# Kernel tuning notes

Hardware: AMD Instinct MI355X
Metric: run time of the kernel (lower is better)

## Reference

```python
import jax, jax.numpy as jnp
import numpy as np

B, T, C = 4, 2048, 1024
N_HEAD = 16
HEAD = C // N_HEAD  # 64


def _rope_tables(T, dim, base=10000.0):
    inv_freq = 1.0 / (base ** (jnp.arange(0, dim, 2, dtype=jnp.float32) / dim))
    t = jnp.arange(T, dtype=jnp.float32)
    freqs = jnp.einsum('i,j->ij', t, inv_freq)           # [T, dim/2]
    emb = jnp.concatenate([freqs, freqs], axis=-1)        # [T, dim]
    return jnp.cos(emb), jnp.sin(emb)                     # each [T, dim]


def _rotate_half(x):
    x1, x2 = x[..., : x.shape[-1] // 2], x[..., x.shape[-1] // 2:]
    return jnp.concatenate([-x2, x1], axis=-1)


def setup_inputs() -> dict:
    key = jax.random.key(0)
    ks = jax.random.split(key, 4)
    x = jax.random.normal(ks[0], (B, T, C), dtype=jnp.float32)
    w_attn = jax.random.normal(ks[1], (C, 3 * C), dtype=jnp.float32) * (1.0 / np.sqrt(C))
    b_attn = jnp.zeros((3 * C,), dtype=jnp.float32)
    w_proj = jax.random.normal(ks[2], (C, C), dtype=jnp.float32) * (1.0 / np.sqrt(C))
    b_proj = jnp.zeros((C,), dtype=jnp.float32)
    return {"x": x, "w_attn": w_attn, "b_attn": b_attn, "w_proj": w_proj, "b_proj": b_proj}


def reference(x, w_attn, b_attn, w_proj, b_proj):
    Bx, Tx, Cx = x.shape
    qkv = x @ w_attn + b_attn                             # [B,T,3C]
    q, k, v = jnp.split(qkv, 3, axis=-1)
    # [B,T,C] -> [B,H,T,hd]
    def to_heads(t):
        return t.reshape(Bx, Tx, N_HEAD, HEAD).transpose(0, 2, 1, 3)
    q, k, v = to_heads(q), to_heads(k), to_heads(v)
    cos, sin = _rope_tables(Tx, HEAD)                     # [T,hd]
    cos = cos[None, None, :, :]
    sin = sin[None, None, :, :]
    q = q * cos + _rotate_half(q) * sin
    k = k * cos + _rotate_half(k) * sin
    scale = 1.0 / np.sqrt(HEAD)
    att = jnp.einsum('bhqd,bhkd->bhqk', q, k) * scale     # [B,H,T,T]
    causal = jnp.tril(jnp.ones((Tx, Tx), dtype=bool))
    att = jnp.where(causal[None, None], att, -jnp.inf)
    att = jax.nn.softmax(att, axis=-1)
    y = jnp.einsum('bhqk,bhkd->bhqd', att, v)             # [B,H,T,hd]
    y = y.transpose(0, 2, 1, 3).reshape(Bx, Tx, Cx)
    return y @ w_proj + b_proj
```

## Files before the change

### kernel.cpp

```cpp
#include <hip/hip_runtime.h>

#define B_  4
#define T_  2048
#define C_  1024
#define NH_ 16
#define HD_ 64
#define BT_ (B_*T_)
#define N3C (3*C_)

typedef _Float16 f16;
typedef _Float16 half8 __attribute__((ext_vector_type(8)));
typedef _Float16 half4 __attribute__((ext_vector_type(4)));
typedef float f32x4 __attribute__((ext_vector_type(4)));

__device__ __forceinline__ void gld16(const f16* g, f16* l) {
  __builtin_amdgcn_global_load_lds(
      (const __attribute__((address_space(1))) unsigned int*)g,
      (__attribute__((address_space(3))) unsigned int*)l, 16, 0, 0);
}

__global__ __launch_bounds__(256) void prep(
    const float* __restrict__ X, f16* __restrict__ X16,
    const float* __restrict__ Wa, f16* __restrict__ Wta,
    const float* __restrict__ Wp, f16* __restrict__ Wtp,
    float2* __restrict__ cs)
{
  __shared__ float Ls[64][65];
  const int tid = threadIdx.x;
  const int blk = blockIdx.x;
  if (blk < 4096) {
    const int i = blk * 256 + tid;
    const float4 a = ((const float4*)X)[i * 2];
    const float4 b = ((const float4*)X)[i * 2 + 1];
    half8 hx;
    hx[0] = (f16)a.x; hx[1] = (f16)a.y; hx[2] = (f16)a.z; hx[3] = (f16)a.w;
    hx[4] = (f16)b.x; hx[5] = (f16)b.y; hx[6] = (f16)b.z; hx[7] = (f16)b.w;
    ((half8*)X16)[i] = hx;
    return;
  }
  if (blk >= 5120) {
    const int i = (blk - 5120) * 256 + tid;
    const int f = i & 31, t = i >> 5;
    const float inv = expf(-(2.0f * (float)f / 64.0f) * 9.210340371976184f);
    float sn, cn;
    sincosf((float)t * inv, &sn, &cn);
    cs[i] = make_float2(cn, sn);
    return;
  }
  const float* W; f16* Wt; int N, i2;
  if (blk < 4864) { W = Wa; Wt = Wta; N = N3C; i2 = blk - 4096; }
  else            { W = Wp; Wt = Wtp; N = C_;  i2 = blk - 4864; }
  const int nblk = N >> 6;
  const int n0 = (i2 % nblk) * 64, k0 = (i2 / nblk) * 64;
#pragma unroll
  for (int j = 0; j < 4; ++j) {
    const int idx = j * 256 + tid;
    const int r = idx >> 4, c = (idx & 15) * 4;
    const float4 w = *(const float4*)(W + (size_t)(k0 + r) * N + n0 + c);
    Ls[r][c + 0] = w.x; Ls[r][c + 1] = w.y; Ls[r][c + 2] = w.z; Ls[r][c + 3] = w.w;
  }
  __syncthreads();
#pragma unroll
  for (int j = 0; j < 2; ++j) {
    const int idx = j * 256 + tid;
    const int r = idx >> 3, c = (idx & 7) * 8;
    half8 hw;
#pragma unroll
    for (int u = 0; u < 8; ++u) hw[u] = (f16)Ls[c + u][r];
    *(half8*)(Wt + (size_t)(n0 + r) * C_ + k0 + c) = hw;
  }
}

__global__ __launch_bounds__(256) void gemm_qkv(
    const f16* __restrict__ A, const f16* __restrict__ Bt,
    const float* __restrict__ bias, const float2* __restrict__ cs,
    f16* __restrict__ Qo, f16* __restrict__ Ko, f16* __restrict__ Vt_g)
{
  __shared__ f16 As[128 * 64];
  __shared__ f16 Bs[128 * 64];
  const int tid  = threadIdx.x;
  const int row0 = blockIdx.y * 128;
  const int col0 = blockIdx.x * 128;
  const int wave = tid >> 6, lane = tid & 63;
  const int l = lane & 15, quad = lane >> 4;
  const int wm = wave >> 1, wn = wave & 1;
  const int sr = tid >> 3;
  const int scs = ((tid & 7) ^ (sr & 7)) * 8;
  const int lq7 = l & 7;

  f32x4 acc[4][4];
#pragma unroll
  for (int mi = 0; mi < 4; ++mi)
#pragma unroll
    for (int ni = 0; ni < 4; ++ni) acc[mi][ni] = (f32x4)0.0f;

  for (int k0 = 0; k0 < C_; k0 += 64) {
    __syncthreads();
#pragma unroll
    for (int p = 0; p < 4; ++p) {
      const int r = p * 32 + sr;
      gld16(A  + (size_t)(row0 + r) * C_ + k0 + scs, &As[p * 2048 + tid * 8]);
      gld16(Bt + (size_t)(col0 + r) * C_ + k0 + scs, &Bs[p * 2048 + tid * 8]);
    }
    __syncthreads();

#pragma unroll
    for (int s = 0; s < 2; ++s) {
      half8 af[4], bf[4];
#pragma unroll
      for (int mi = 0; mi < 4; ++mi)
        af[mi] = *(const half8*)&As[(wm * 64 + mi * 16 + l) * 64 + ((((s << 2) | quad) ^ lq7) << 3)];
#pragma unroll
      for (int ni = 0; ni < 4; ++ni)
        bf[ni] = *(const half8*)&Bs[(wn * 64 + ni * 16 + l) * 64 + ((((s << 2) | quad) ^ lq7) << 3)];
#pragma unroll
      for (int mi = 0; mi < 4; ++mi)
#pragma unroll
        for (int ni = 0; ni < 4; ++ni)
          acc[mi][ni] = __builtin_amdgcn_mfma_f32_16x16x32_f16(af[mi], bf[ni], acc[mi][ni], 0, 0, 0);
    }
  }

  const int region = col0 >> 10;
  const int colw = col0 + wn * 64;
  const int h = (colw & 1023) >> 6;
  if (region < 2) {
    f16* dst = (region == 0) ? Qo : Ko;
    const float qs = (region == 0) ? 0.18033688f : 1.0f;
#pragma unroll
    for (int mi = 0; mi < 4; ++mi) {
#pragma unroll
      for (int r = 0; r < 4; ++r) {
        const int gm = row0 + wm * 64 + mi * 16 + quad * 4 + r;
        const int b = gm >> 11, t = gm & (T_ - 1);
        const size_t base = ((size_t)(b * NH_ + h) * T_ + t) * HD_;
        const float2* csrow = cs + t * 32;
#pragma unroll
        for (int ni = 0; ni < 2; ++ni) {
          const int d = ni * 16 + l;
          const float2 c2 = csrow[d];
          const float x1 = acc[mi][ni][r]     + bias[colw + d];
          const float x2 = acc[mi][ni + 2][r] + bias[colw + d + 32];
          dst[base + d]      = (f16)((x1 * c2.x - x2 * c2.y) * qs);
          dst[base + d + 32] = (f16)((x2 * c2.x + x1 * c2.y) * qs);
        }
      }
    }
  } else {
#pragma unroll
    for (int mi = 0; mi < 4; ++mi) {
      const int t0 = row0 + wm * 64 + mi * 16 + quad * 4;
      const int b = t0 >> 11, t = t0 & (T_ - 1);
#pragma unroll
      for (int ni = 0; ni < 4; ++ni) {
        const int d = ni * 16 + l;
        const float bs = bias[colw + d];
        half4 o;
#pragma unroll
        for (int r = 0; r < 4; ++r) o[r] = (f16)(acc[mi][ni][r] + bs);
        *(half4*)(Vt_g + ((size_t)((b * NH_ + h) * HD_ + d)) * T_ + t) = o;
      }
    }
  }
}

__global__ __launch_bounds__(256) void attn_mfma(
    const f16* __restrict__ Qg, const f16* __restrict__ Kg,
    const f16* __restrict__ Vt_g, f16* __restrict__ Y)
{
  __shared__ f16 Ks[2][64 * 64];
  __shared__ f16 Vt[2][64 * 64];
  const int tid  = threadIdx.x;
  const int qt   = 15 - (blockIdx.x >> 6);
  const int bh   = blockIdx.x & 63;
  const int b    = bh >> 4, h = bh & 15;
  const int wave = tid >> 6, lane = tid & 63;
  const int l    = lane & 15, quad = lane >> 4;
  const int lq7  = l & 7;
  int qrow[2];
  qrow[0] = qt * 128 + wave * 16 + l;
  qrow[1] = qrow[0] + 64;

  half8 qf[2][2];
#pragma unroll
  for (int u = 0; u < 2; ++u) {
    const f16* qp = Qg + ((size_t)bh * T_ + qrow[u]) * HD_;
#pragma unroll
    for (int s = 0; s < 2; ++s)
      qf[u][s] = *(const half8*)(qp + s * 32 + quad * 8);
  }

  f32x4 O[2][4];
#pragma unroll
  for (int u = 0; u < 2; ++u)
#pragma unroll
    for (int mi = 0; mi < 4; ++mi) O[u][mi] = (f32x4)0.0f;
  float l_run[2] = {0.f, 0.f};

  const f16* kbase  = Kg   + (size_t)bh * T_ * HD_;
  const f16* vtbase = Vt_g + (size_t)bh * HD_ * T_;
  const int r0 = tid >> 3, cc = tid & 7;

  const int nkt = 2 * qt + 2;
  half8 hk[2], hv[2];
#pragma unroll
  for (int i = 0; i < 2; ++i) {
    const int r = i * 32 + r0;
    hk[i] = *(const half8*)(kbase + (size_t)r * HD_ + cc * 8);
    hv[i] = *(const half8*)(vtbase + (size_t)r * T_ + cc * 8);
  }

  for (int kt = 0; kt < nkt; ++kt) {
    f16* KsB = Ks[kt & 1];
    f16* VtB = Vt[kt & 1];
#pragma unroll
    for (int i = 0; i < 2; ++i) {
      const int r = i * 32 + r0;
      const int cst = ((cc ^ (r & 7)) << 3);
      *(half8*)&KsB[r * 64 + cst] = hk[i];
      *(half8*)&VtB[r * 64 + cst] = hv[i];
    }
    __syncthreads();
    if (kt + 1 < nkt) {
#pragma unroll
      for (int i = 0; i < 2; ++i) {
        const int r = i * 32 + r0;
        hk[i] = *(const half8*)(kbase + (size_t)((kt + 1) * 64 + r) * HD_ + cc * 8);
        hv[i] = *(const half8*)(vtbase + (size_t)r * T_ + (kt + 1) * 64 + cc * 8);
      }
    }

    f32x4 St[2][4];
#pragma unroll
    for (int u = 0; u < 2; ++u)
#pragma unroll
      for (int st = 0; st < 4; ++st) St[u][st] = (f32x4)0.0f;
#pragma unroll
    for (int st = 0; st < 4; ++st) {
#pragma unroll
      for (int s = 0; s < 2; ++s) {
        const int row = st * 16 + l;
        const half8 af = *(const half8*)&KsB[row * 64 + ((((s << 2) | quad) ^ lq7) << 3)];
#pragma unroll
        for (int u = 0; u < 2; ++u)
          St[u][st] = __builtin_amdgcn_mfma_f32_16x16x32_f16(af, qf[u][s], St[u][st], 0, 0, 0);
      }
    }

    const bool domask = (kt >= 2 * qt);
    const int k0 = kt * 64;
    half4 pf[2][4];
#pragma unroll
    for (int u = 0; u < 2; ++u) {
      float psum = 0.f;
#pragma unroll
      for (int st = 0; st < 4; ++st) {
        float pv[4];
#pragma unroll
        for (int r = 0; r < 4; ++r) {
          float x = St[u][st][r];
          if (domask) {
            const int key = k0 + st * 16 + quad * 4 + r;
            if (key > qrow[u]) x = -1e9f;
          }
          const float ev = exp2f(x);
          pv[r] = ev;
          psum += ev;
        }
        pf[u][st][0] = (f16)pv[0]; pf[u][st][1] = (f16)pv[1];
        pf[u][st][2] = (f16)pv[2]; pf[u][st][3] = (f16)pv[3];
      }
      l_run[u] += psum;
    }

#pragma unroll
    for (int mi = 0; mi < 4; ++mi) {
      const int row = mi * 16 + l;
#pragma unroll
      for (int ki = 0; ki < 4; ++ki) {
        const int kch = (ki << 1) | (quad >> 1);
        const half4 vf = *(const half4*)&VtB[row * 64 + ((kch ^ lq7) << 3) + ((quad & 1) << 2)];
#pragma unroll
        for (int u = 0; u < 2; ++u)
          O[u][mi] = __builtin_amdgcn_mfma_f32_16x16x16f16(vf, pf[u][ki], O[u][mi], 0, 0, 0);
      }
    }
  }

#pragma unroll
  for (int u = 0; u < 2; ++u) {
    float lt = l_run[u];
    lt += __shfl_xor(lt, 16);
    lt += __shfl_xor(lt, 32);
    const float inv = 1.0f / lt;
    f16* yp = Y + ((size_t)(b * T_) + qrow[u]) * C_ + h * 64;
#pragma unroll
    for (int mi = 0; mi < 4; ++mi) {
      half4 o;
      o[0] = (f16)(O[u][mi][0] * inv); o[1] = (f16)(O[u][mi][1] * inv);
      o[2] = (f16)(O[u][mi][2] * inv); o[3] = (f16)(O[u][mi][3] * inv);
      *(half4*)(yp + mi * 16 + quad * 4) = o;
    }
  }
}

__global__ __launch_bounds__(256) void gemm_proj(
    const f16* __restrict__ A, const f16* __restrict__ Bt,
    const float* __restrict__ bias, float* __restrict__ Out)
{
  __shared__ f16 As[128 * 64];
  __shared__ f16 Bs[128 * 64];
  const int tid  = threadIdx.x;
  const int row0 = blockIdx.y * 128;
  const int col0 = blockIdx.x * 128;
  const int wave = tid >> 6, lane = tid & 63;
  const int l = lane & 15, quad = lane >> 4;
  const int wm = wave >> 1, wn = wave & 1;
  const int sr = tid >> 3;
  const int scs = ((tid & 7) ^ (sr & 7)) * 8;
  const int lq7 = l & 7;

  f32x4 acc[4][4];
#pragma unroll
  for (int mi = 0; mi < 4; ++mi)
#pragma unroll
    for (int ni = 0; ni < 4; ++ni) acc[mi][ni] = (f32x4)0.0f;

  for (int k0 = 0; k0 < C_; k0 += 64) {
    __syncthreads();
#pragma unroll
    for (int p = 0; p < 4; ++p) {
      const int r = p * 32 + sr;
      gld16(A  + (size_t)(row0 + r) * C_ + k0 + scs, &As[p * 2048 + tid * 8]);
      gld16(Bt + (size_t)(col0 + r) * C_ + k0 + scs, &Bs[p * 2048 + tid * 8]);
    }
    __syncthreads();

#pragma unroll
    for (int s = 0; s < 2; ++s) {
      half8 af[4], bf[4];
#pragma unroll
      for (int mi = 0; mi < 4; ++mi)
        af[mi] = *(const half8*)&As[(wm * 64 + mi * 16 + l) * 64 + ((((s << 2) | quad) ^ lq7) << 3)];
#pragma unroll
      for (int ni = 0; ni < 4; ++ni)
        bf[ni] = *(const half8*)&Bs[(wn * 64 + ni * 16 + l) * 64 + ((((s << 2) | quad) ^ lq7) << 3)];
#pragma unroll
      for (int mi = 0; mi < 4; ++mi)
#pragma unroll
        for (int ni = 0; ni < 4; ++ni)
          acc[mi][ni] = __builtin_amdgcn_mfma_f32_16x16x32_f16(af[mi], bf[ni], acc[mi][ni], 0, 0, 0);
    }
  }

#pragma unroll
  for (int mi = 0; mi < 4; ++mi) {
#pragma unroll
    for (int ni = 0; ni < 4; ++ni) {
#pragma unroll
      for (int r = 0; r < 4; ++r) {
        const int gm = row0 + wm * 64 + mi * 16 + quad * 4 + r;
        const int n  = col0 + wn * 64 + ni * 16 + l;
        Out[(size_t)gm * C_ + n] = acc[mi][ni][r] + bias[n];
      }
    }
  }
}

extern "C" void kernel_launch(void* const* d_in, const int* in_sizes, int n_in,
                              void* d_out, int out_size, void* d_ws, size_t ws_size,
                              hipStream_t stream) {
  const float* x      = (const float*)d_in[0];
  const float* w_attn = (const float*)d_in[1];
  const float* b_attn = (const float*)d_in[2];
  const float* w_proj = (const float*)d_in[3];
  const float* b_proj = (const float*)d_in[4];
  float* out = (float*)d_out;

  const size_t elems = (size_t)BT_ * C_;
  f16* x16 = (f16*)d_ws;
  f16* wta = x16 + elems;
  f16* wtp = wta + (size_t)N3C * C_;
  f16* q   = wtp + (size_t)C_ * C_;
  f16* k   = q + elems;
  f16* vt  = k + elems;
  f16* y   = vt + elems;
  float2* cs = (float2*)(y + elems);

  prep<<<dim3(5376), 256, 0, stream>>>(x, x16, w_attn, wta, w_proj, wtp, cs);
  gemm_qkv<<<dim3(N3C / 128, BT_ / 128), 256, 0, stream>>>(x16, wta, b_attn, cs, q, k, vt);
  attn_mfma<<<dim3(16 * 64), 256, 0, stream>>>(q, k, vt, y);
  gemm_proj<<<dim3(C_ / 128, BT_ / 128), 256, 0, stream>>>(y, wtp, b_proj, out);
}
```

Baseline: 272.3 us.

## Pair complementary 64-row query tiles per block for causal load balance

Each attention block now handles two 64-row query tiles (tiles pr and 31-pr) in sequence instead of one 128-row tile, so every block does about the same number of causal key tiles. Block indices are remapped so consecutive blocks spread across different (batch, head) pairs, likely with XCD placement in mind. In exchange, each loaded K/V tile now feeds 64 queries instead of 128, which doubles the K/V reloads and halves the MFMA work per LDS read, and a barrier is added between the two passes.

```diff
diff --git a/kernel.cpp b/kernel.cpp
--- a/kernel.cpp
+++ b/kernel.cpp
@@ -171,134 +171,126 @@
   __shared__ f16 Ks[2][64 * 64];
   __shared__ f16 Vt[2][64 * 64];
   const int tid  = threadIdx.x;
-  const int qt   = 15 - (blockIdx.x >> 6);
-  const int bh   = blockIdx.x & 63;
+  const int w    = (blockIdx.x & 7) * 128 + (blockIdx.x >> 3);
+  const int bh   = w >> 4;
+  const int pr   = w & 15;
   const int b    = bh >> 4, h = bh & 15;
   const int wave = tid >> 6, lane = tid & 63;
   const int l    = lane & 15, quad = lane >> 4;
   const int lq7  = l & 7;
-  int qrow[2];
-  qrow[0] = qt * 128 + wave * 16 + l;
-  qrow[1] = qrow[0] + 64;
-
-  half8 qf[2][2];
-#pragma unroll
-  for (int u = 0; u < 2; ++u) {
-    const f16* qp = Qg + ((size_t)bh * T_ + qrow[u]) * HD_;
-#pragma unroll
-    for (int s = 0; s < 2; ++s)
-      qf[u][s] = *(const half8*)(qp + s * 32 + quad * 8);
-  }
-
-  f32x4 O[2][4];
-#pragma unroll
-  for (int u = 0; u < 2; ++u)
-#pragma unroll
-    for (int mi = 0; mi < 4; ++mi) O[u][mi] = (f32x4)0.0f;
-  float l_run[2] = {0.f, 0.f};
+  const int r0   = tid >> 3, cc = tid & 7;
 
   const f16* kbase  = Kg   + (size_t)bh * T_ * HD_;
   const f16* vtbase = Vt_g + (size_t)bh * HD_ * T_;
-  const int r0 = tid >> 3, cc = tid & 7;
-
-  const int nkt = 2 * qt + 2;
-  half8 hk[2], hv[2];
-#pragma unroll
-  for (int i = 0; i < 2; ++i) {
-    const int r = i * 32 + r0;
-    hk[i] = *(const half8*)(kbase + (size_t)r * HD_ + cc * 8);
-    hv[i] = *(const half8*)(vtbase + (size_t)r * T_ + cc * 8);
-  }
-
-  for (int kt = 0; kt < nkt; ++kt) {
-    f16* KsB = Ks[kt & 1];
-    f16* VtB = Vt[kt & 1];
+
+  const int qts[2] = { 31 - pr, pr };
+
+#pragma unroll 1
+  for (int pass = 0; pass < 2; ++pass) {
+    const int qt   = qts[pass];
+    const int nkt  = qt + 1;
+    const int qrow = qt * 64 + wave * 16 + l;
+
+    half8 qf[2];
+    {
+      const f16* qp = Qg + ((size_t)bh * T_ + qrow) * HD_;
+      qf[0] = *(const half8*)(qp + quad * 8);
+      qf[1] = *(const half8*)(qp + 32 + quad * 8);
+    }
+
+    f32x4 O[4];
+#pragma unroll
+    for (int mi = 0; mi < 4; ++mi) O[mi] = (f32x4)0.0f;
+    float l_run = 0.f;
+
+    half8 hk[2], hv[2];
 #pragma unroll
     for (int i = 0; i < 2; ++i) {
       const int r = i * 32 + r0;
-      const int cst = ((cc ^ (r & 7)) << 3);
-      *(half8*)&KsB[r * 64 + cst] = hk[i];
-      *(half8*)&VtB[r * 64 + cst] = hv[i];
-    }
-    __syncthreads();
-    if (kt + 1 < nkt) {
+      hk[i] = *(const half8*)(kbase + (size_t)r * HD_ + cc * 8);
+      hv[i] = *(const half8*)(vtbase + (size_t)r * T_ + cc * 8);
+    }
+
+    if (pass == 1) __syncthreads();
+
+    for (int kt = 0; kt < nkt; ++kt) {
+      f16* KsB = Ks[kt & 1];
+      f16* VtB = Vt[kt & 1];
 #pragma unroll
       for (int i = 0; i < 2; ++i) {
         const int r = i * 32 + r0;
-        hk[i] = *(const half8*)(kbase + (size_t)((kt + 1) * 64 + r) * HD_ + cc * 8);
-        hv[i] = *(const half8*)(vtbase + (size_t)r * T_ + (kt + 1) * 64 + cc * 8);
-      }
-    }
-
-    f32x4 St[2][4];
-#pragma unroll
-    for (int u = 0; u < 2; ++u)
-#pragma unroll
-      for (int st = 0; st < 4; ++st) St[u][st] = (f32x4)0.0f;
-#pragma unroll
-    for (int st = 0; st < 4; ++st) {
-#pragma unroll
-      for (int s = 0; s < 2; ++s) {
-        const int row = st * 16 + l;
-        const half8 af = *(const half8*)&KsB[row * 64 + ((((s << 2) | quad) ^ lq7) << 3)];
-#pragma unroll
-        for (int u = 0; u < 2; ++u)
-          St[u][st] = __builtin_amdgcn_mfma_f32_16x16x32_f16(af, qf[u][s], St[u][st], 0, 0, 0);
-      }
-    }
-
-    const bool domask = (kt >= 2 * qt);
-    const int k0 = kt * 64;
-    half4 pf[2][4];
-#pragma unroll
-    for (int u = 0; u < 2; ++u) {
+        const int cst = ((cc ^ (r & 7)) << 3);
+        *(half8*)&KsB[r * 64 + cst] = hk[i];
+        *(half8*)&VtB[r * 64 + cst] = hv[i];
+      }
+      __syncthreads();
+      if (kt + 1 < nkt) {
+#pragma unroll
+        for (int i = 0; i < 2; ++i) {
+          const int r = i * 32 + r0;
+          hk[i] = *(const half8*)(kbase + (size_t)((kt + 1) * 64 + r) * HD_ + cc * 8);
+          hv[i] = *(const half8*)(vtbase + (size_t)r * T_ + (kt + 1) * 64 + cc * 8);
+        }
+      }
+
+      f32x4 St[4];
+#pragma unroll
+      for (int st = 0; st < 4; ++st) St[st] = (f32x4)0.0f;
+#pragma unroll
+      for (int st = 0; st < 4; ++st) {
+#pragma unroll
+        for (int s = 0; s < 2; ++s) {
+          const int row = st * 16 + l;
+          const half8 af = *(const half8*)&KsB[row * 64 + ((((s << 2) | quad) ^ lq7) << 3)];
+          St[st] = __builtin_amdgcn_mfma_f32_16x16x32_f16(af, qf[s], St[st], 0, 0, 0);
+        }
+      }
+
+      const bool domask = (kt == qt);
+      const int k0 = kt * 64;
+      half4 pf[4];
       float psum = 0.f;
 #pragma unroll
       for (int st = 0; st < 4; ++st) {
         float pv[4];
 #pragma unroll
         for (int r = 0; r < 4; ++r) {
-          float x = St[u][st][r];
+          float x = St[st][r];
           if (domask) {
             const int key = k0 + st * 16 + quad * 4 + r;
-            if (key > qrow[u]) x = -1e9f;
+            if (key > qrow) x = -1e9f;
           }
           const float ev = exp2f(x);
           pv[r] = ev;
           psum += ev;
         }
-        pf[u][st][0] = (f16)pv[0]; pf[u][st][1] = (f16)pv[1];
-        pf[u][st][2] = (f16)pv[2]; pf[u][st][3] = (f16)pv[3];
-      }
-      l_run[u] += psum;
-    }
-
-#pragma unroll
-    for (int mi = 0; mi < 4; ++mi) {
-      const int row = mi * 16 + l;
-#pragma unroll
-      for (int ki = 0; ki < 4; ++ki) {
-        const int kch = (ki << 1) | (quad >> 1);
-        const half4 vf = *(const half4*)&VtB[row * 64 + ((kch ^ lq7) << 3) + ((quad & 1) << 2)];
-#pragma unroll
-        for (int u = 0; u < 2; ++u)
-          O[u][mi] = __builtin_amdgcn_mfma_f32_16x16x16f16(vf, pf[u][ki], O[u][mi], 0, 0, 0);
-      }
-    }
-  }
-
-#pragma unroll
-  for (int u = 0; u < 2; ++u) {
-    float lt = l_run[u];
+        pf[st][0] = (f16)pv[0]; pf[st][1] = (f16)pv[1];
+        pf[st][2] = (f16)pv[2]; pf[st][3] = (f16)pv[3];
+      }
+      l_run += psum;
+
+#pragma unroll
+      for (int mi = 0; mi < 4; ++mi) {
+        const int row = mi * 16 + l;
+#pragma unroll
+        for (int ki = 0; ki < 4; ++ki) {
+          const int kch = (ki << 1) | (quad >> 1);
+          const half4 vf = *(const half4*)&VtB[row * 64 + ((kch ^ lq7) << 3) + ((quad & 1) << 2)];
+          O[mi] = __builtin_amdgcn_mfma_f32_16x16x16f16(vf, pf[ki], O[mi], 0, 0, 0);
+        }
+      }
+    }
+
+    float lt = l_run;
     lt += __shfl_xor(lt, 16);
     lt += __shfl_xor(lt, 32);
     const float inv = 1.0f / lt;
-    f16* yp = Y + ((size_t)(b * T_) + qrow[u]) * C_ + h * 64;
+    f16* yp = Y + ((size_t)(b * T_) + qrow) * C_ + h * 64;
 #pragma unroll
     for (int mi = 0; mi < 4; ++mi) {
       half4 o;
-      o[0] = (f16)(O[u][mi][0] * inv); o[1] = (f16)(O[u][mi][1] * inv);
-      o[2] = (f16)(O[u][mi][2] * inv); o[3] = (f16)(O[u][mi][3] * inv);
+      o[0] = (f16)(O[mi][0] * inv); o[1] = (f16)(O[mi][1] * inv);
+      o[2] = (f16)(O[mi][2] * inv); o[3] = (f16)(O[mi][3] * inv);
       *(half4*)(yp + mi * 16 + quad * 4) = o;
     }
   }
@@ -389,6 +381,6 @@
 
   prep<<<dim3(5376), 256, 0, stream>>>(x, x16, w_attn, wta, w_proj, wtp, cs);
   gemm_qkv<<<dim3(N3C / 128, BT_ / 128), 256, 0, stream>>>(x16, wta, b_attn, cs, q, k, vt);
-  attn_mfma<<<dim3(16 * 64), 256, 0, stream>>>(q, k, vt, y);
+  attn_mfma<<<dim3(1024), 256, 0, stream>>>(q, k, vt, y);
   gemm_proj<<<dim3(C_ / 128, BT_ / 128), 256, 0, stream>>>(y, wtp, b_proj, out);
 }
```

New measurement: 278.7 us. 1.02x slower.

## Pair complementary causal query tiles per block to balance attention work

Applied to the files above, without the earlier changes.

Each attention block now handles two 64-row query tiles, pr and 31-pr, instead of one contiguous 128-row tile. This gives every block the same number of key tiles, and the second tile's MFMAs are skipped once past its causal limit. Block indices are also remapped with an XCD-style interleave (blockIdx&7) so blocks from the same head are grouped. This targets load imbalance and tail effects from causal masking, at the cost of extra branching inside the loop and lower Q-tile reuse in later iterations.

```diff
diff --git a/kernel.cpp b/kernel.cpp
--- a/kernel.cpp
+++ b/kernel.cpp
@@ -171,23 +171,27 @@
   __shared__ f16 Ks[2][64 * 64];
   __shared__ f16 Vt[2][64 * 64];
   const int tid  = threadIdx.x;
-  const int qt   = 15 - (blockIdx.x >> 6);
-  const int bh   = blockIdx.x & 63;
+  const int w    = (blockIdx.x & 7) * 128 + (blockIdx.x >> 3);
+  const int bh   = w >> 4;
+  const int pr   = w & 15;
+  const int qta  = 31 - pr;
+  const int qtb  = pr;
   const int b    = bh >> 4, h = bh & 15;
   const int wave = tid >> 6, lane = tid & 63;
   const int l    = lane & 15, quad = lane >> 4;
   const int lq7  = l & 7;
+  const int r0   = tid >> 3, cc = tid & 7;
+
   int qrow[2];
-  qrow[0] = qt * 128 + wave * 16 + l;
-  qrow[1] = qrow[0] + 64;
+  qrow[0] = qta * 64 + wave * 16 + l;
+  qrow[1] = qtb * 64 + wave * 16 + l;
 
   half8 qf[2][2];
 #pragma unroll
   for (int u = 0; u < 2; ++u) {
     const f16* qp = Qg + ((size_t)bh * T_ + qrow[u]) * HD_;
-#pragma unroll
-    for (int s = 0; s < 2; ++s)
-      qf[u][s] = *(const half8*)(qp + s * 32 + quad * 8);
+    qf[u][0] = *(const half8*)(qp + quad * 8);
+    qf[u][1] = *(const half8*)(qp + 32 + quad * 8);
   }
 
   f32x4 O[2][4];
@@ -199,9 +203,8 @@
 
   const f16* kbase  = Kg   + (size_t)bh * T_ * HD_;
   const f16* vtbase = Vt_g + (size_t)bh * HD_ * T_;
-  const int r0 = tid >> 3, cc = tid & 7;
-
-  const int nkt = 2 * qt + 2;
+
+  const int nkt = qta + 1;
   half8 hk[2], hv[2];
 #pragma unroll
   for (int i = 0; i < 2; ++i) {
@@ -211,6 +214,7 @@
   }
 
   for (int kt = 0; kt < nkt; ++kt) {
+    const bool dual = (kt <= qtb);
     f16* KsB = Ks[kt & 1];
     f16* VtB = Vt[kt & 1];
 #pragma unroll
@@ -241,17 +245,18 @@
       for (int s = 0; s < 2; ++s) {
         const int row = st * 16 + l;
         const half8 af = *(const half8*)&KsB[row * 64 + ((((s << 2) | quad) ^ lq7) << 3)];
-#pragma unroll
-        for (int u = 0; u < 2; ++u)
-          St[u][st] = __builtin_amdgcn_mfma_f32_16x16x32_f16(af, qf[u][s], St[u][st], 0, 0, 0);
-      }
-    }
-
-    const bool domask = (kt >= 2 * qt);
+        St[0][st] = __builtin_amdgcn_mfma_f32_16x16x32_f16(af, qf[0][s], St[0][st], 0, 0, 0);
+        if (dual)
+          St[1][st] = __builtin_amdgcn_mfma_f32_16x16x32_f16(af, qf[1][s], St[1][st], 0, 0, 0);
+      }
+    }
+
     const int k0 = kt * 64;
     half4 pf[2][4];
 #pragma unroll
     for (int u = 0; u < 2; ++u) {
+      if (u == 1 && !dual) continue;
+      const bool domask = (kt == (u == 0 ? qta : qtb));
       float psum = 0.f;
 #pragma unroll
       for (int st = 0; st < 4; ++st) {
@@ -280,9 +285,9 @@
       for (int ki = 0; ki < 4; ++ki) {
         const int kch = (ki << 1) | (quad >> 1);
         const half4 vf = *(const half4*)&VtB[row * 64 + ((kch ^ lq7) << 3) + ((quad & 1) << 2)];
-#pragma unroll
-        for (int u = 0; u < 2; ++u)
-          O[u][mi] = __builtin_amdgcn_mfma_f32_16x16x16f16(vf, pf[u][ki], O[u][mi], 0, 0, 0);
+        O[0][mi] = __builtin_amdgcn_mfma_f32_16x16x16f16(vf, pf[0][ki], O[0][mi], 0, 0, 0);
+        if (dual)
+          O[1][mi] = __builtin_amdgcn_mfma_f32_16x16x16f16(vf, pf[1][ki], O[1][mi], 0, 0, 0);
       }
     }
   }
@@ -389,6 +394,6 @@
 
   prep<<<dim3(5376), 256, 0, stream>>>(x, x16, w_attn, wta, w_proj, wtp, cs);
   gemm_qkv<<<dim3(N3C / 128, BT_ / 128), 256, 0, stream>>>(x16, wta, b_attn, cs, q, k, vt);
-  attn_mfma<<<dim3(16 * 64), 256, 0, stream>>>(q, k, vt, y);
+  attn_mfma<<<dim3(1024), 256, 0, stream>>>(q, k, vt, y);
   gemm_proj<<<dim3(C_ / 128, BT_ / 128), 256, 0, stream>>>(y, wtp, b_proj, out);
 }
```

Measured after the change: 306.3 us. 1.13x slower.

## Pair causal query tiles per attention block and stage V-transpose stores through LDS

Applied to the files above, without the earlier changes.

The attention kernel now launches 512 blocks, and each block handles two query tiles (qt and 15-qt) one after the other. Every block therefore does the same amount of causal work, which removes the tail caused by unequal blocks. Block indices are also remapped so that blocks sharing a batch-head are spread out. In the QKV GEMM, the V-transposed output is written to a swizzled shared-memory tile first and then stored to global memory as coalesced 16-byte rows, instead of scattered 8-byte writes. The cost is an extra LDS round trip and barriers in the V path, plus fewer, longer attention blocks, which may lower occupancy and latency hiding.

```diff
diff --git a/kernel.cpp b/kernel.cpp
--- a/kernel.cpp
+++ b/kernel.cpp
@@ -76,8 +76,9 @@
     const float* __restrict__ bias, const float2* __restrict__ cs,
     f16* __restrict__ Qo, f16* __restrict__ Ko, f16* __restrict__ Vt_g)
 {
-  __shared__ f16 As[128 * 64];
-  __shared__ f16 Bs[128 * 64];
+  __shared__ f16 S[16384];
+  f16* As = S;
+  f16* Bs = S + 8192;
   const int tid  = threadIdx.x;
   const int row0 = blockIdx.y * 128;
   const int col0 = blockIdx.x * 128;
@@ -147,10 +148,12 @@
       }
     }
   } else {
+    __syncthreads();
+    const int bloc  = row0 >> 11;
+    const int tbase = row0 & (T_ - 1);
 #pragma unroll
     for (int mi = 0; mi < 4; ++mi) {
-      const int t0 = row0 + wm * 64 + mi * 16 + quad * 4;
-      const int b = t0 >> 11, t = t0 & (T_ - 1);
+      const int t_loc = wm * 64 + mi * 16 + quad * 4;
 #pragma unroll
       for (int ni = 0; ni < 4; ++ni) {
         const int d = ni * 16 + l;
@@ -158,8 +161,21 @@
         half4 o;
 #pragma unroll
         for (int r = 0; r < 4; ++r) o[r] = (f16)(acc[mi][ni][r] + bs);
-        *(half4*)(Vt_g + ((size_t)((b * NH_ + h) * HD_ + d)) * T_ + t) = o;
-      }
+        const int ts = t_loc ^ ((d & 15) << 3);
+        *(half4*)&S[wn * 8192 + d * 128 + ts] = o;
+      }
+    }
+    __syncthreads();
+#pragma unroll
+    for (int j = 0; j < 8; ++j) {
+      const int flat = j * 256 + tid;
+      const int buf  = flat >> 10;
+      const int rem  = flat & 1023;
+      const int d    = rem >> 4;
+      const int tt   = (rem & 15) << 3;
+      const half8 v  = *(const half8*)&S[buf * 8192 + d * 128 + (tt ^ ((d & 15) << 3))];
+      const int hh   = ((col0 + buf * 64) & 1023) >> 6;
+      *(half8*)(Vt_g + ((size_t)((bloc * NH_ + hh) * HD_ + d)) * T_ + tbase + tt) = v;
     }
   }
 }
@@ -171,135 +187,145 @@
   __shared__ f16 Ks[2][64 * 64];
   __shared__ f16 Vt[2][64 * 64];
   const int tid  = threadIdx.x;
-  const int qt   = 15 - (blockIdx.x >> 6);
-  const int bh   = blockIdx.x & 63;
+  const int w    = (blockIdx.x & 7) * 64 + (blockIdx.x >> 3);
+  const int bh   = w >> 3;
+  const int ppr  = w & 7;
   const int b    = bh >> 4, h = bh & 15;
   const int wave = tid >> 6, lane = tid & 63;
   const int l    = lane & 15, quad = lane >> 4;
   const int lq7  = l & 7;
-  int qrow[2];
-  qrow[0] = qt * 128 + wave * 16 + l;
-  qrow[1] = qrow[0] + 64;
-
-  half8 qf[2][2];
-#pragma unroll
-  for (int u = 0; u < 2; ++u) {
-    const f16* qp = Qg + ((size_t)bh * T_ + qrow[u]) * HD_;
-#pragma unroll
-    for (int s = 0; s < 2; ++s)
-      qf[u][s] = *(const half8*)(qp + s * 32 + quad * 8);
-  }
-
-  f32x4 O[2][4];
-#pragma unroll
-  for (int u = 0; u < 2; ++u)
-#pragma unroll
-    for (int mi = 0; mi < 4; ++mi) O[u][mi] = (f32x4)0.0f;
-  float l_run[2] = {0.f, 0.f};
+  const int r0   = tid >> 3, cc = tid & 7;
 
   const f16* kbase  = Kg   + (size_t)bh * T_ * HD_;
   const f16* vtbase = Vt_g + (size_t)bh * HD_ * T_;
-  const int r0 = tid >> 3, cc = tid & 7;
-
-  const int nkt = 2 * qt + 2;
-  half8 hk[2], hv[2];
-#pragma unroll
-  for (int i = 0; i < 2; ++i) {
-    const int r = i * 32 + r0;
-    hk[i] = *(const half8*)(kbase + (size_t)r * HD_ + cc * 8);
-    hv[i] = *(const half8*)(vtbase + (size_t)r * T_ + cc * 8);
-  }
-
-  for (int kt = 0; kt < nkt; ++kt) {
-    f16* KsB = Ks[kt & 1];
-    f16* VtB = Vt[kt & 1];
+
+  const int qts[2] = { 15 - ppr, ppr };
+
+#pragma unroll 1
+  for (int pass = 0; pass < 2; ++pass) {
+    const int qt  = qts[pass];
+    const int nkt = 2 * qt + 2;
+    int qrow[2];
+    qrow[0] = qt * 128 + wave * 16 + l;
+    qrow[1] = qrow[0] + 64;
+
+    half8 qf[2][2];
+#pragma unroll
+    for (int u = 0; u < 2; ++u) {
+      const f16* qp = Qg + ((size_t)bh * T_ + qrow[u]) * HD_;
+#pragma unroll
+      for (int s = 0; s < 2; ++s)
+        qf[u][s] = *(const half8*)(qp + s * 32 + quad * 8);
+    }
+
+    f32x4 O[2][4];
+#pragma unroll
+    for (int u = 0; u < 2; ++u)
+#pragma unroll
+      for (int mi = 0; mi < 4; ++mi) O[u][mi] = (f32x4)0.0f;
+    float l_run[2] = {0.f, 0.f};
+
+    half8 hk[2], hv[2];
 #pragma unroll
     for (int i = 0; i < 2; ++i) {
       const int r = i * 32 + r0;
-      const int cst = ((cc ^ (r & 7)) << 3);
-      *(half8*)&KsB[r * 64 + cst] = hk[i];
-      *(half8*)&VtB[r * 64 + cst] = hv[i];
-    }
-    __syncthreads();
-    if (kt + 1 < nkt) {
+      hk[i] = *(const half8*)(kbase + (size_t)r * HD_ + cc * 8);
+      hv[i] = *(const half8*)(vtbase + (size_t)r * T_ + cc * 8);
+    }
+
+    if (pass == 1) __syncthreads();
+
+    for (int kt = 0; kt < nkt; ++kt) {
+      f16* KsB = Ks[kt & 1];
+      f16* VtB = Vt[kt & 1];
 #pragma unroll
       for (int i = 0; i < 2; ++i) {
         const int r = i * 32 + r0;
-        hk[i] = *(const half8*)(kbase + (size_t)((kt + 1) * 64 + r) * HD_ + cc * 8);
-        hv[i] = *(const half8*)(vtbase + (size_t)r * T_ + (kt + 1) * 64 + cc * 8);
-      }
-    }
-
-    f32x4 St[2][4];
-#pragma unroll
-    for (int u = 0; u < 2; ++u)
-#pragma unroll
-      for (int st = 0; st < 4; ++st) St[u][st] = (f32x4)0.0f;
-#pragma unroll
-    for (int st = 0; st < 4; ++st) {
-#pragma unroll
-      for (int s = 0; s < 2; ++s) {
-        const int row = st * 16 + l;
-        const half8 af = *(const half8*)&KsB[row * 64 + ((((s << 2) | quad) ^ lq7) << 3)];
-#pragma unroll
-        for (int u = 0; u < 2; ++u)
-          St[u][st] = __builtin_amdgcn_mfma_f32_16x16x32_f16(af, qf[u][s], St[u][st], 0, 0, 0);
-      }
-    }
-
-    const bool domask = (kt >= 2 * qt);
-    const int k0 = kt * 64;
-    half4 pf[2][4];
+        const int cst = ((cc ^ (r & 7)) << 3);
+        *(half8*)&KsB[r * 64 + cst] = hk[i];
+        *(half8*)&VtB[r * 64 + cst] = hv[i];
+      }
+      __syncthreads();
+      if (kt + 1 < nkt) {
+#pragma unroll
+        for (int i = 0; i < 2; ++i) {
+          const int r = i * 32 + r0;
+          hk[i] = *(const half8*)(kbase + (size_t)((kt + 1) * 64 + r) * HD_ + cc * 8);
+          hv[i] = *(const half8*)(vtbase + (size_t)r * T_ + (kt + 1) * 64 + cc * 8);
+        }
+      }
+
+      f32x4 St[2][4];
+#pragma unroll
+      for (int u = 0; u < 2; ++u)
+#pragma unroll
+        for (int st = 0; st < 4; ++st) St[u][st] = (f32x4)0.0f;
+#pragma unroll
+      for (int st = 0; st < 4; ++st) {
+#pragma unroll
+        for (int s = 0; s < 2; ++s) {
+          const int row = st * 16 + l;
+          const half8 af = *(const half8*)&KsB[row * 64 + ((((s << 2) | quad) ^ lq7) << 3)];
+#pragma unroll
+          for (int u = 0; u < 2; ++u)
+            St[u][st] = __builtin_amdgcn_mfma_f32_16x16x32_f16(af, qf[u][s], St[u][st], 0, 0, 0);
+        }
+      }
+
+      const bool domask = (kt >= 2 * qt);
+      const int k0 = kt * 64;
+      half4 pf[2][4];
+#pragma unroll
+      for (int u = 0; u < 2; ++u) {
+        float psum = 0.f;
+#pragma unroll
+        for (int st = 0; st < 4; ++st) {
+          float pv[4];
+#pragma unroll
+          for (int r = 0; r < 4; ++r) {
+            float x = St[u][st][r];
+            if (domask) {
+              const int key = k0 + st * 16 + quad * 4 + r;
+              if (key > qrow[u]) x = -1e9f;
+            }
+            const float ev = exp2f(x);
+            pv[r] = ev;
+            psum += ev;
+          }
+          pf[u][st][0] = (f16)pv[0]; pf[u][st][1] = (f16)pv[1];
+          pf[u][st][2] = (f16)pv[2]; pf[u][st][3] = (f16)pv[3];
+        }
+        l_run[u] += psum;
+      }
+
+#pragma unroll
+      for (int mi = 0; mi < 4; ++mi) {
+        const int row = mi * 16 + l;
+#pragma unroll
+        for (int ki = 0; ki < 4; ++ki) {
+          const int kch = (ki << 1) | (quad >> 1);
+          const half4 vf = *(const half4*)&VtB[row * 64 + ((kch ^ lq7) << 3) + ((quad & 1) << 2)];
+#pragma unroll
+          for (int u = 0; u < 2; ++u)
+            O[u][mi] = __builtin_amdgcn_mfma_f32_16x16x16f16(vf, pf[u][ki], O[u][mi], 0, 0, 0);
+        }
+      }
+    }
+
 #pragma unroll
     for (int u = 0; u < 2; ++u) {
-      float psum = 0.f;
-#pragma unroll
-      for (int st = 0; st < 4; ++st) {
-        float pv[4];
-#pragma unroll
-        for (int r = 0; r < 4; ++r) {
-          float x = St[u][st][r];
-          if (domask) {
-            const int key = k0 + st * 16 + quad * 4 + r;
-            if (key > qrow[u]) x = -1e9f;
-          }
-          const float ev = exp2f(x);
-          pv[r] = ev;
-          psum += ev;
-        }
-        pf[u][st][0] = (f16)pv[0]; pf[u][st][1] = (f16)pv[1];
-        pf[u][st][2] = (f16)pv[2]; pf[u][st][3] = (f16)pv[3];
-      }
-      l_run[u] += psum;
-    }
-
-#pragma unroll
-    for (int mi = 0; mi < 4; ++mi) {
-      const int row = mi * 16 + l;
-#pragma unroll
-      for (int ki = 0; ki < 4; ++ki) {
-        const int kch = (ki << 1) | (quad >> 1);
-        const half4 vf = *(const half4*)&VtB[row * 64 + ((kch ^ lq7) << 3) + ((quad & 1) << 2)];
-#pragma unroll
-        for (int u = 0; u < 2; ++u)
-          O[u][mi] = __builtin_amdgcn_mfma_f32_16x16x16f16(vf, pf[u][ki], O[u][mi], 0, 0, 0);
-      }
-    }
-  }
-
-#pragma unroll
-  for (int u = 0; u < 2; ++u) {
-    float lt = l_run[u];
-    lt += __shfl_xor(lt, 16);
-    lt += __shfl_xor(lt, 32);
-    const float inv = 1.0f / lt;
-    f16* yp = Y + ((size_t)(b * T_) + qrow[u]) * C_ + h * 64;
-#pragma unroll
-    for (int mi = 0; mi < 4; ++mi) {
-      half4 o;
-      o[0] = (f16)(O[u][mi][0] * inv); o[1] = (f16)(O[u][mi][1] * inv);
-      o[2] = (f16)(O[u][mi][2] * inv); o[3] = (f16)(O[u][mi][3] * inv);
-      *(half4*)(yp + mi * 16 + quad * 4) = o;
+      float lt = l_run[u];
+      lt += __shfl_xor(lt, 16);
+      lt += __shfl_xor(lt, 32);
+      const float inv = 1.0f / lt;
+      f16* yp = Y + ((size_t)(b * T_) + qrow[u]) * C_ + h * 64;
+#pragma unroll
+      for (int mi = 0; mi < 4; ++mi) {
+        half4 o;
+        o[0] = (f16)(O[u][mi][0] * inv); o[1] = (f16)(O[u][mi][1] * inv);
+        o[2] = (f16)(O[u][mi][2] * inv); o[3] = (f16)(O[u][mi][3] * inv);
+        *(half4*)(yp + mi * 16 + quad * 4) = o;
+      }
     }
   }
 }
@@ -389,6 +415,6 @@
 
   prep<<<dim3(5376), 256, 0, stream>>>(x, x16, w_attn, wta, w_proj, wtp, cs);
   gemm_qkv<<<dim3(N3C / 128, BT_ / 128), 256, 0, stream>>>(x16, wta, b_attn, cs, q, k, vt);
-  attn_mfma<<<dim3(16 * 64), 256, 0, stream>>>(q, k, vt, y);
+  attn_mfma<<<dim3(512), 256, 0, stream>>>(q, k, vt, y);
   gemm_proj<<<dim3(C_ / 128, BT_ / 128), 256, 0, stream>>>(y, wtp, b_proj, out);
 }
```

Result: no change. 275.6 us (+1.2%).
